# Optimization experiments

Measured on AMD Instinct MI355X. Metric: run time of the kernel, lower is better.

Reference implementation:

```python
import jax, jax.numpy as jnp
import numpy as np

N, D, K, G = 262144, 256, 1024, 4
C = D // G
BETA = 0.5


def setup_inputs() -> dict:
    key = jax.random.key(0)
    k1, k2 = jax.random.split(key)
    z = jax.random.normal(k1, (N, D), dtype=jnp.float32)
    # original init: uniform(-1/K, 1/K)
    codebooks = jax.random.uniform(k2, (G, K, C), dtype=jnp.float32,
                                   minval=-1.0 / K, maxval=1.0 / K)
    return {"z": z, "codebooks": codebooks}


def reference(z, codebooks):
    # z: [N, D] -> [N, G, C]; codebooks: [G, K, C]
    zg = z.reshape(-1, G, C)
    # squared distances: ||z||^2 + ||e||^2 - 2 z.e  -> [N, G, K]
    z_sq = jnp.sum(zg ** 2, axis=-1, keepdims=True)            # [N, G, 1]
    e_sq = jnp.sum(codebooks ** 2, axis=-1)                    # [G, K]
    dots = jnp.einsum('ngc,gkc->ngk', zg, codebooks)           # [N, G, K]
    d = z_sq + e_sq[None, :, :] - 2.0 * dots
    idx = jnp.argmin(d, axis=-1)                               # [N, G]
    # gather codes: [N, G, C]
    zq = codebooks[jnp.arange(G)[None, :], idx]
    # per-group VQ loss, averaged over groups (means over N and C per group)
    sg = jax.lax.stop_gradient
    commit = jnp.mean((sg(zq) - zg) ** 2, axis=(0, 2))         # [G]
    embed = jnp.mean((zq - sg(zg)) ** 2, axis=(0, 2))          # [G]
    loss = jnp.mean(BETA * commit + embed)
    # straight-through estimator
    zq_st = zg + sg(zq - zg)
    return zq_st.reshape(-1, D), loss
```

## Files before the change

kernel.cpp:

```cpp
#include <hip/hip_runtime.h>
#include <hip/hip_fp16.h>
#include <stdint.h>

typedef _Float16 f16;
typedef f16   f16x8 __attribute__((ext_vector_type(8)));
typedef float f32x4 __attribute__((ext_vector_type(4)));

#define NTOK 262144
#define DDIM 256
#define KCB  1024
#define GG   4
#define CC   64
#define FR   8

static __device__ __forceinline__ uint32_t umin32(uint32_t a, uint32_t b) { return a < b ? a : b; }

__global__ __launch_bounds__(64) void vq_prep(const float* __restrict__ cb,
                                              f16* __restrict__ cb16,
                                              float* __restrict__ esq05,
                                              float* __restrict__ loss_acc) {
    int gk = blockIdx.x;
    int c  = threadIdx.x;
    float v = cb[(size_t)gk * CC + c];
    cb16[(size_t)gk * CC + c] = (f16)v;
    float s = v * v;
    #pragma unroll
    for (int off = 32; off; off >>= 1) s += __shfl_down(s, off, 64);
    if (c == 0) esq05[gk] = 0.5f + s;
    if (gk == 0 && c == 0) *loss_acc = 0.0f;
}

__global__ __launch_bounds__(256) void vq_main(const float* __restrict__ z,
                                               const float* __restrict__ cb32,
                                               const f16* __restrict__ cb16,
                                               const float* __restrict__ esq05,
                                               float* __restrict__ out,
                                               float* __restrict__ loss_acc) {
    const int lane = threadIdx.x & 63;
    const int w    = threadIdx.x >> 6;
    const int g    = blockIdx.y;
    const int r0   = blockIdx.x * (FR * 16 * 4) + w * (FR * 16);
    const int q    = lane >> 4;
    const int t    = lane & 15;

    f16x8 a[FR][2];
    float zsq[FR];
    #pragma unroll
    for (int f = 0; f < FR; ++f) {
        int row = r0 + f * 16 + t;
        const float* zp = z + (size_t)row * DDIM + g * CC + q * 8;
        float4 v0 = *(const float4*)(zp);
        float4 v1 = *(const float4*)(zp + 4);
        float4 v2 = *(const float4*)(zp + 32);
        float4 v3 = *(const float4*)(zp + 36);
        f16x8 a0 = { (f16)(-2.f*v0.x),(f16)(-2.f*v0.y),(f16)(-2.f*v0.z),(f16)(-2.f*v0.w),
                     (f16)(-2.f*v1.x),(f16)(-2.f*v1.y),(f16)(-2.f*v1.z),(f16)(-2.f*v1.w) };
        f16x8 a1 = { (f16)(-2.f*v2.x),(f16)(-2.f*v2.y),(f16)(-2.f*v2.z),(f16)(-2.f*v2.w),
                     (f16)(-2.f*v3.x),(f16)(-2.f*v3.y),(f16)(-2.f*v3.z),(f16)(-2.f*v3.w) };
        a[f][0] = a0; a[f][1] = a1;
        float s = v0.x*v0.x + v0.y*v0.y + v0.z*v0.z + v0.w*v0.w
                + v1.x*v1.x + v1.y*v1.y + v1.z*v1.z + v1.w*v1.w
                + v2.x*v2.x + v2.y*v2.y + v2.z*v2.z + v2.w*v2.w
                + v3.x*v3.x + v3.y*v3.y + v3.z*v3.z + v3.w*v3.w;
        s += __shfl_xor(s, 16, 64);
        s += __shfl_xor(s, 32, 64);
        zsq[f] = s;
    }

    uint32_t run[FR][4];
    #pragma unroll
    for (int f = 0; f < FR; ++f)
        #pragma unroll
        for (int i = 0; i < 4; ++i) run[f][i] = 0xFFFFFFFFu;

    const f16*   cbg = cb16  + (size_t)g * KCB * CC;
    const float* eg  = esq05 + (size_t)g * KCB;

    f16x8 b0c, b1c; float ec;
    {
        const f16x8* bp = (const f16x8*)(cbg + (size_t)t * CC + q * 8);
        b0c = bp[0]; b1c = bp[4]; ec = eg[t];
    }

    for (int n0 = 0; n0 < KCB; n0 += 16) {
        int nn = (n0 + 16) & (KCB - 1);
        const f16x8* nbp = (const f16x8*)(cbg + (size_t)(nn + t) * CC + q * 8);
        f16x8 nb0 = nbp[0];
        f16x8 nb1 = nbp[4];
        float ne  = eg[nn + t];

        uint32_t code = (uint32_t)(n0 + t);
        f32x4 ce = { ec, ec, ec, ec };
        #pragma unroll
        for (int f = 0; f < FR; ++f) {
            f32x4 acc = __builtin_amdgcn_mfma_f32_16x16x32_f16(a[f][0], b0c, ce, 0, 0, 0);
            acc = __builtin_amdgcn_mfma_f32_16x16x32_f16(a[f][1], b1c, acc, 0, 0, 0);
            #pragma unroll
            for (int i = 0; i < 4; ++i) {
                uint32_t key = (__float_as_uint(acc[i]) & 0xFFFFFC00u) | code;
                run[f][i] = umin32(run[f][i], key);
            }
        }
        b0c = nb0; b1c = nb1; ec = ne;
    }

    float lsum = 0.0f;
    #pragma unroll
    for (int f = 0; f < FR; ++f) {
        #pragma unroll
        for (int i = 0; i < 4; ++i) {
            uint32_t k = run[f][i];
            k = umin32(k, __shfl_xor(k, 1, 64));
            k = umin32(k, __shfl_xor(k, 2, 64));
            k = umin32(k, __shfl_xor(k, 4, 64));
            k = umin32(k, __shfl_xor(k, 8, 64));
            int   kw     = (int)(k & 1023u);
            float minval = __uint_as_float(k & 0xFFFFFC00u) - 0.5f;
            int rloc = q * 4 + i;
            int grow = r0 + f * 16 + rloc;
            const float4* src = (const float4*)(cb32 + ((size_t)(g * KCB + kw)) * CC) + t;
            float4*       dst = (float4*)(out + (size_t)grow * DDIM + g * CC) + t;
            *dst = *src;
            float zs = __shfl(zsq[f], rloc, 64);
            if (t == 0) lsum += zs + minval;
        }
    }
    #pragma unroll
    for (int off = 32; off; off >>= 1) lsum += __shfl_down(lsum, off, 64);
    if (lane == 0) atomicAdd(loss_acc, lsum);
}

__global__ void vq_final(const float* __restrict__ loss_acc, float* __restrict__ out_loss) {
    *out_loss = 1.5f * (*loss_acc) * (1.0f / ((float)NTOK * (float)DDIM));
}

extern "C" void kernel_launch(void* const* d_in, const int* in_sizes, int n_in,
                              void* d_out, int out_size, void* d_ws, size_t ws_size,
                              hipStream_t stream) {
    const float* z  = (const float*)d_in[0];
    const float* cb = (const float*)d_in[1];
    float* out = (float*)d_out;

    char* ws = (char*)d_ws;
    f16*   cb16     = (f16*)ws;
    float* esq05    = (float*)(ws + (size_t)GG * KCB * CC * sizeof(f16));
    float* loss_acc = (float*)(ws + (size_t)GG * KCB * CC * sizeof(f16)
                                  + (size_t)GG * KCB * sizeof(float));

    vq_prep<<<GG * KCB, 64, 0, stream>>>(cb, cb16, esq05, loss_acc);

    dim3 grid(NTOK / (FR * 16 * 4), GG);
    vq_main<<<grid, 256, 0, stream>>>(z, cb, cb16, esq05, out, loss_acc);

    vq_final<<<1, 1, 0, stream>>>(loss_acc, out + (size_t)NTOK * DDIM);
}
```

Before: 262.0 us.

## Halve row tile, process two codebook tiles per step, replace atomic loss with partials

Each wave now handles 4 row fragments instead of 8, but each loop iteration processes 32 codebook entries as two independent 16-wide MFMA chains. This reorganizes the A/B reuse and adds instruction-level parallelism, and the launch-bounds hint requests higher occupancy. The global atomicAdd for the loss is replaced by per-block partial sums that a 256-thread final kernel reduces. This doubles the grid size and the codebook reads per row, and the final reduction now runs over many more partial values.

New measurement: 325.7 us. +24.3%, slower.

```diff
diff --git a/kernel.cpp b/kernel.cpp
--- a/kernel.cpp
+++ b/kernel.cpp
@@ -11,14 +11,15 @@
 #define KCB  1024
 #define GG   4
 #define CC   64
-#define FR   8
+#define FR   4
+#define NBLKX (NTOK / (FR * 16 * 4))
+#define NPART (NBLKX * GG)
 
 static __device__ __forceinline__ uint32_t umin32(uint32_t a, uint32_t b) { return a < b ? a : b; }
 
 __global__ __launch_bounds__(64) void vq_prep(const float* __restrict__ cb,
                                               f16* __restrict__ cb16,
-                                              float* __restrict__ esq05,
-                                              float* __restrict__ loss_acc) {
+                                              float* __restrict__ esq05) {
     int gk = blockIdx.x;
     int c  = threadIdx.x;
     float v = cb[(size_t)gk * CC + c];
@@ -27,15 +28,14 @@
     #pragma unroll
     for (int off = 32; off; off >>= 1) s += __shfl_down(s, off, 64);
     if (c == 0) esq05[gk] = 0.5f + s;
-    if (gk == 0 && c == 0) *loss_acc = 0.0f;
 }
 
-__global__ __launch_bounds__(256) void vq_main(const float* __restrict__ z,
-                                               const float* __restrict__ cb32,
-                                               const f16* __restrict__ cb16,
-                                               const float* __restrict__ esq05,
-                                               float* __restrict__ out,
-                                               float* __restrict__ loss_acc) {
+__global__ __launch_bounds__(256, 4) void vq_main(const float* __restrict__ z,
+                                                  const float* __restrict__ cb32,
+                                                  const f16* __restrict__ cb16,
+                                                  const float* __restrict__ esq05,
+                                                  float* __restrict__ out,
+                                                  float* __restrict__ part) {
     const int lane = threadIdx.x & 63;
     const int w    = threadIdx.x >> 6;
     const int g    = blockIdx.y;
@@ -76,32 +76,41 @@
     const f16*   cbg = cb16  + (size_t)g * KCB * CC;
     const float* eg  = esq05 + (size_t)g * KCB;
 
-    f16x8 b0c, b1c; float ec;
+    f16x8 cb0A, cb1A, cb0B, cb1B; float ceA, ceB;
     {
         const f16x8* bp = (const f16x8*)(cbg + (size_t)t * CC + q * 8);
-        b0c = bp[0]; b1c = bp[4]; ec = eg[t];
+        cb0A = bp[0];  cb1A = bp[4];
+        cb0B = bp[128]; cb1B = bp[132];
+        ceA = eg[t]; ceB = eg[16 + t];
     }
 
-    for (int n0 = 0; n0 < KCB; n0 += 16) {
-        int nn = (n0 + 16) & (KCB - 1);
+    for (int n0 = 0; n0 < KCB; n0 += 32) {
+        int nn = (n0 + 32) & (KCB - 1);
         const f16x8* nbp = (const f16x8*)(cbg + (size_t)(nn + t) * CC + q * 8);
-        f16x8 nb0 = nbp[0];
-        f16x8 nb1 = nbp[4];
-        float ne  = eg[nn + t];
+        f16x8 nb0A = nbp[0];
+        f16x8 nb1A = nbp[4];
+        f16x8 nb0B = nbp[128];
+        f16x8 nb1B = nbp[132];
+        float neA  = eg[nn + t];
+        float neB  = eg[nn + 16 + t];
 
-        uint32_t code = (uint32_t)(n0 + t);
-        f32x4 ce = { ec, ec, ec, ec };
+        uint32_t codeA = (uint32_t)(n0 + t);
+        f32x4 cqA = { ceA, ceA, ceA, ceA };
+        f32x4 cqB = { ceB, ceB, ceB, ceB };
         #pragma unroll
         for (int f = 0; f < FR; ++f) {
-            f32x4 acc = __builtin_amdgcn_mfma_f32_16x16x32_f16(a[f][0], b0c, ce, 0, 0, 0);
-            acc = __builtin_amdgcn_mfma_f32_16x16x32_f16(a[f][1], b1c, acc, 0, 0, 0);
+            f32x4 accA = __builtin_amdgcn_mfma_f32_16x16x32_f16(a[f][0], cb0A, cqA, 0, 0, 0);
+            accA = __builtin_amdgcn_mfma_f32_16x16x32_f16(a[f][1], cb1A, accA, 0, 0, 0);
+            f32x4 accB = __builtin_amdgcn_mfma_f32_16x16x32_f16(a[f][0], cb0B, cqB, 0, 0, 0);
+            accB = __builtin_amdgcn_mfma_f32_16x16x32_f16(a[f][1], cb1B, accB, 0, 0, 0);
             #pragma unroll
             for (int i = 0; i < 4; ++i) {
-                uint32_t key = (__float_as_uint(acc[i]) & 0xFFFFFC00u) | code;
-                run[f][i] = umin32(run[f][i], key);
+                uint32_t kA = (__float_as_uint(accA[i]) & 0xFFFFFC00u) | codeA;
+                uint32_t kB = (__float_as_uint(accB[i]) & 0xFFFFFC00u) | (codeA + 16);
+                run[f][i] = umin32(run[f][i], umin32(kA, kB));
             }
         }
-        b0c = nb0; b1c = nb1; ec = ne;
+        cb0A = nb0A; cb1A = nb1A; cb0B = nb0B; cb1B = nb1B; ceA = neA; ceB = neB;
     }
 
     float lsum = 0.0f;
@@ -127,11 +136,28 @@
     }
     #pragma unroll
     for (int off = 32; off; off >>= 1) lsum += __shfl_down(lsum, off, 64);
-    if (lane == 0) atomicAdd(loss_acc, lsum);
+
+    __shared__ float ls[4];
+    if (lane == 0) ls[w] = lsum;
+    __syncthreads();
+    if (threadIdx.x == 0) {
+        part[blockIdx.y * NBLKX + blockIdx.x] = ls[0] + ls[1] + ls[2] + ls[3];
+    }
 }
 
-__global__ void vq_final(const float* __restrict__ loss_acc, float* __restrict__ out_loss) {
-    *out_loss = 1.5f * (*loss_acc) * (1.0f / ((float)NTOK * (float)DDIM));
+__global__ __launch_bounds__(256) void vq_final(const float* __restrict__ part,
+                                                float* __restrict__ out_loss) {
+    __shared__ float ls[4];
+    float s = 0.0f;
+    for (int i = threadIdx.x; i < NPART; i += 256) s += part[i];
+    #pragma unroll
+    for (int off = 32; off; off >>= 1) s += __shfl_down(s, off, 64);
+    int lane = threadIdx.x & 63, w = threadIdx.x >> 6;
+    if (lane == 0) ls[w] = s;
+    __syncthreads();
+    if (threadIdx.x == 0) {
+        *out_loss = 1.5f * (ls[0] + ls[1] + ls[2] + ls[3]) * (1.0f / ((float)NTOK * (float)DDIM));
+    }
 }
 
 extern "C" void kernel_launch(void* const* d_in, const int* in_sizes, int n_in,
@@ -142,15 +168,15 @@
     float* out = (float*)d_out;
 
     char* ws = (char*)d_ws;
-    f16*   cb16     = (f16*)ws;
-    float* esq05    = (float*)(ws + (size_t)GG * KCB * CC * sizeof(f16));
-    float* loss_acc = (float*)(ws + (size_t)GG * KCB * CC * sizeof(f16)
-                                  + (size_t)GG * KCB * sizeof(float));
+    f16*   cb16  = (f16*)ws;
+    float* esq05 = (float*)(ws + (size_t)GG * KCB * CC * sizeof(f16));
+    float* part  = (float*)(ws + (size_t)GG * KCB * CC * sizeof(f16)
+                               + (size_t)GG * KCB * sizeof(float));
 
-    vq_prep<<<GG * KCB, 64, 0, stream>>>(cb, cb16, esq05, loss_acc);
+    vq_prep<<<GG * KCB, 64, 0, stream>>>(cb, cb16, esq05);
 
-    dim3 grid(NTOK / (FR * 16 * 4), GG);
-    vq_main<<<grid, 256, 0, stream>>>(z, cb, cb16, esq05, out, loss_acc);
+    dim3 grid(NBLKX, GG);
+    vq_main<<<grid, 256, 0, stream>>>(z, cb, cb16, esq05, out, part);
 
-    vq_final<<<1, 1, 0, stream>>>(loss_acc, out + (size_t)NTOK * DDIM);
+    vq_final<<<1, 256, 0, stream>>>(part, out + (size_t)NTOK * DDIM);
 }
```
